# Performance work log

Hardware: AMD Instinct MI355X
Metric: run time of the kernel (lower is better)

Reference implementation:

```python
import jax, jax.numpy as jnp
import numpy as np

N = 8192
NFEAT = 512
NHID = 512
NCLASS = 64
NLAYERS = 8
LAMDA = 0.5
ALPHA = 0.1
EDGE_P = 0.002  # ~16 avg degree


def setup_inputs() -> dict:
    key = jax.random.key(0)
    ks = jax.random.split(key, 6)
    x = jax.random.normal(ks[0], (N, NFEAT), dtype=jnp.float32)
    # sparse 0/1 adjacency, densified (the original densifies adj each layer)
    adj = (jax.random.uniform(ks[1], (N, N)) < EDGE_P).astype(jnp.float32)
    stdv1 = 1.0 / np.sqrt(NHID)
    fc1_W = jax.random.normal(ks[2], (NFEAT, NHID), dtype=jnp.float32) * stdv1
    fc1_b = jnp.zeros((NHID,), dtype=jnp.float32)
    # GraphConvolution.reset_parameters: uniform(-1/sqrt(out), 1/sqrt(out))
    conv_Ws = jax.random.uniform(ks[3], (NLAYERS, NHID, NHID), minval=-stdv1, maxval=stdv1, dtype=jnp.float32)
    stdv2 = 1.0 / np.sqrt(NCLASS)
    fc2_W = jax.random.normal(ks[4], (NHID, NCLASS), dtype=jnp.float32) * stdv2
    fc2_b = jnp.zeros((NCLASS,), dtype=jnp.float32)
    return {"x": x, "adj": adj, "fc1_W": fc1_W, "fc1_b": fc1_b,
            "conv_Ws": conv_Ws, "fc2_W": fc2_W, "fc2_b": fc2_b}


def reference(x, adj, fc1_W, fc1_b, conv_Ws, fc2_W, fc2_b):
    n = adj.shape[0]
    # A_hat = A + I ; P = D^{-1/2} A_hat D^{-1/2}  (diag matmuls -> row/col scaling)
    A_hat = adj + jnp.eye(n, dtype=adj.dtype)
    dinv = 1.0 / jnp.sqrt(jnp.sum(A_hat, axis=0))  # [N]
    P = dinv[:, None] * A_hat * dinv[None, :]      # identical every layer; compute once

    H0 = jax.nn.relu(x @ fc1_W + fc1_b)            # fc1 (dropout is identity: training=False)
    H = H0
    for i in range(NLAYERS):
        beta = float(np.log(LAMDA / (i + 1) + 1.0))
        init_res = (1.0 - ALPHA) * (P @ H) + ALPHA * H0
        # init_res @ ((1-beta) I + beta W) expanded:
        H = jax.nn.relu((1.0 - beta) * init_res + beta * (init_res @ conv_Ws[i]))
    logits = H @ fc2_W + fc2_b
    return -jax.nn.log_softmax(logits, axis=1)
```

## Files before the change

kernel.cpp:

```cpp
#include <hip/hip_runtime.h>
#include <hip/hip_bf16.h>
#include <cmath>

#define N_NODES 8192
#define NFEAT 512
#define NHID 512
#define NCLASS 64
#define NLAYERS 8
#define CAP 96

typedef __attribute__((ext_vector_type(8))) short bf16x8;
typedef __attribute__((ext_vector_type(4))) float f32x4;
typedef unsigned short u16;

__device__ inline float bf2f(short u) {
  union { unsigned int i; float f; } x;
  x.i = ((unsigned int)(u16)u) << 16;
  return x.f;
}
__device__ inline short f2bf(float f) {
  union { float f; unsigned int i; } x;
  x.f = f;
  unsigned int r = x.i + 0x7FFFu + ((x.i >> 16) & 1u);
  return (short)(r >> 16);
}

__global__ __launch_bounds__(256)
void extract_kernel(const float* __restrict__ adj, int* __restrict__ idx,
                    int* __restrict__ cnt, int* __restrict__ colcnt)
{
  __shared__ int s_cnt;
  const int i = blockIdx.x;
  if (threadIdx.x == 0) s_cnt = 0;
  __syncthreads();
  const uint4* row = (const uint4*)(adj + (size_t)i * N_NODES);
  for (int c = threadIdx.x; c < N_NODES / 4; c += 256) {
    uint4 v = row[c];
    if ((v.x | v.y | v.z | v.w) == 0u) continue;
    unsigned int vals[4] = {v.x, v.y, v.z, v.w};
    #pragma unroll
    for (int e = 0; e < 4; ++e) {
      if (vals[e] != 0u) {
        int p = atomicAdd(&s_cnt, 1);
        if (p < CAP) idx[(size_t)i * CAP + p] = c * 4 + e;
        atomicAdd(&colcnt[c * 4 + e], 1);
      }
    }
  }
  __syncthreads();
  if (threadIdx.x == 0) cnt[i] = min(s_cnt, CAP);
}

__global__ __launch_bounds__(256)
void dinv_kernel(const int* __restrict__ colcnt, float* __restrict__ dinv)
{
  int j = blockIdx.x * 256 + threadIdx.x;
  if (j < N_NODES) dinv[j] = 1.0f / sqrtf((float)colcnt[j] + 1.0f);
}

__global__ __launch_bounds__(256)
void cvt_bf16_kernel(const float* __restrict__ src, u16* __restrict__ dst, int n4)
{
  int i = blockIdx.x * 256 + threadIdx.x;
  if (i >= n4) return;
  float4 v = ((const float4*)src)[i];
  ushort4 o;
  o.x = (u16)f2bf(v.x); o.y = (u16)f2bf(v.y);
  o.z = (u16)f2bf(v.z); o.w = (u16)f2bf(v.w);
  ((ushort4*)dst)[i] = o;
}

__global__ __launch_bounds__(256)
void transpose_cast_kernel(const float* __restrict__ fc1W, const float* __restrict__ convW,
                           u16* __restrict__ Wt)
{
  __shared__ float tile[32][33];
  const int m = blockIdx.z;
  const float* src = (m == 0) ? fc1W : convW + (size_t)(m - 1) * NHID * NHID;
  u16* dst = Wt + (size_t)m * NHID * NHID;
  const int k0 = blockIdx.x * 32, n0 = blockIdx.y * 32;
  const int tx = threadIdx.x & 31, ty = threadIdx.x >> 5;
  #pragma unroll
  for (int r = 0; r < 32; r += 8)
    tile[ty + r][tx] = src[(size_t)(k0 + ty + r) * NHID + n0 + tx];
  __syncthreads();
  #pragma unroll
  for (int r = 0; r < 32; r += 8)
    dst[(size_t)(n0 + ty + r) * NHID + k0 + tx] = (u16)f2bf(tile[tx][ty + r]);
}

#define AS1 __attribute__((address_space(1)))
#define AS3 __attribute__((address_space(3)))

__device__ inline void load16(const void* g, void* l) {
  __builtin_amdgcn_global_load_lds((const AS1 void*)g, (AS3 void*)l, 16, 0, 0);
}

template<int MODE>
__global__ __launch_bounds__(256, 2)
void gemm_kernel(const u16* __restrict__ A, const u16* __restrict__ Bt,
                 const float* __restrict__ bias, const u16* __restrict__ skip,
                 const float* __restrict__ dinv, float cA, float cB,
                 u16* __restrict__ out0, u16* __restrict__ out1)
{
  constexpr int K = 512, N = 512;
  __shared__ u16 ldsA[2][64 * 32];
  __shared__ u16 ldsB[2][128 * 32];
  const int tid = threadIdx.x;
  const int wave = tid >> 6, lane = tid & 63;
  const int m0 = blockIdx.x * 64, n0 = blockIdx.y * 128;
  const int wr = wave >> 1, wc = wave & 1;
  const int lrow = lane & 15, lk = lane >> 4;

  f32x4 acc[2][4];
  #pragma unroll
  for (int a = 0; a < 2; ++a)
    #pragma unroll
    for (int b = 0; b < 4; ++b)
      acc[a][b] = (f32x4){0.f, 0.f, 0.f, 0.f};

  auto stage = [&](int b, int ks) {
    {
      const int c = wave * 64 + lane;
      load16(A + (size_t)(m0 + (c >> 2)) * K + ks + (c & 3) * 8,
             &ldsA[b][(wave * 64) * 8]);
    }
    #pragma unroll
    for (int r = 0; r < 2; ++r) {
      const int c = r * 256 + wave * 64 + lane;
      load16(Bt + (size_t)(n0 + (c >> 2)) * K + ks + (c & 3) * 8,
             &ldsB[b][(r * 256 + wave * 64) * 8]);
    }
  };

  stage(0, 0);
  __syncthreads();

  for (int t = 0; t < 16; ++t) {
    const int b = t & 1;
    if (t + 1 < 16) stage(b ^ 1, (t + 1) * 32);
    bf16x8 af[2], bfr[4];
    #pragma unroll
    for (int mi = 0; mi < 2; ++mi)
      af[mi] = *(const bf16x8*)&ldsA[b][(wr * 32 + mi * 16 + lrow) * 32 + lk * 8];
    #pragma unroll
    for (int ni = 0; ni < 4; ++ni)
      bfr[ni] = *(const bf16x8*)&ldsB[b][(wc * 64 + ni * 16 + lrow) * 32 + lk * 8];
    #pragma unroll
    for (int mi = 0; mi < 2; ++mi)
      #pragma unroll
      for (int ni = 0; ni < 4; ++ni)
        acc[mi][ni] = __builtin_amdgcn_mfma_f32_16x16x32_bf16(af[mi], bfr[ni], acc[mi][ni], 0, 0, 0);
    __syncthreads();
  }

  #pragma unroll
  for (int mi = 0; mi < 2; ++mi) {
    #pragma unroll
    for (int ni = 0; ni < 4; ++ni) {
      #pragma unroll
      for (int r = 0; r < 4; ++r) {
        const int row = m0 + wr * 32 + mi * 16 + lk * 4 + r;
        const int col = n0 + wc * 64 + ni * 16 + lrow;
        const size_t o = (size_t)row * N + col;
        float v = acc[mi][ni][r];
        if (MODE == 0) {
          v = fmaxf(v + bias[col], 0.f);
          out0[o] = (u16)f2bf(v);
          out1[o] = (u16)f2bf(dinv[row] * v);
        } else {
          v = fmaxf(cA * bf2f((short)skip[o]) + cB * v, 0.f);
          out0[o] = (u16)f2bf(MODE == 1 ? dinv[row] * v : v);
        }
      }
    }
  }
}

__global__ __launch_bounds__(256)
void spmm_kernel(const u16* __restrict__ Hs, const u16* __restrict__ H0,
                 const float* __restrict__ dinv, const int* __restrict__ idx,
                 const int* __restrict__ cnt, u16* __restrict__ IR)
{
  const int wave = threadIdx.x >> 6, lane = threadIdx.x & 63;
  const int i = blockIdx.x * 4 + wave;
  const int c0 = lane * 8;
  const int n = cnt[i];
  int jreg = 0;
  if (lane < n) jreg = idx[(size_t)i * CAP + lane] & (N_NODES - 1);

  float acc[8];
  #pragma unroll
  for (int e = 0; e < 8; ++e) acc[e] = 0.f;

  const int nn = min(n, 64);
  int t = 0;
  for (; t + 8 <= nn; t += 8) {
    bf16x8 v[8];
    #pragma unroll
    for (int u = 0; u < 8; ++u) {
      const int j = __shfl(jreg, t + u);
      v[u] = *(const bf16x8*)&Hs[(size_t)j * NHID + c0];
    }
    #pragma unroll
    for (int u = 0; u < 8; ++u)
      #pragma unroll
      for (int e = 0; e < 8; ++e)
        acc[e] += bf2f(v[u][e]);
  }
  for (; t < nn; ++t) {
    const int j = __shfl(jreg, t);
    bf16x8 v = *(const bf16x8*)&Hs[(size_t)j * NHID + c0];
    #pragma unroll
    for (int e = 0; e < 8; ++e) acc[e] += bf2f(v[e]);
  }
  for (; t < n; ++t) {
    const int j = idx[(size_t)i * CAP + t] & (N_NODES - 1);
    bf16x8 v = *(const bf16x8*)&Hs[(size_t)j * NHID + c0];
    #pragma unroll
    for (int e = 0; e < 8; ++e) acc[e] += bf2f(v[e]);
  }

  const float di = dinv[i];
  bf16x8 self = *(const bf16x8*)&Hs[(size_t)i * NHID + c0];
  bf16x8 h0   = *(const bf16x8*)&H0[(size_t)i * NHID + c0];
  bf16x8 ov;
  #pragma unroll
  for (int e = 0; e < 8; ++e) {
    float v = 0.9f * di * (acc[e] + bf2f(self[e])) + 0.1f * bf2f(h0[e]);
    ov[e] = f2bf(v);
  }
  *(bf16x8*)&IR[(size_t)i * NHID + c0] = ov;
}

__global__ __launch_bounds__(256)
void fc2_softmax_kernel(const u16* __restrict__ H, const float* __restrict__ W,
                        const float* __restrict__ b, float* __restrict__ out)
{
  __shared__ float sh[4][4][512];
  const int wave = threadIdx.x >> 6, lane = threadIdx.x & 63;
  const int rowBase = blockIdx.x * 16 + wave * 4;
  #pragma unroll
  for (int rr = 0; rr < 4; ++rr) {
    bf16x8 hv = *(const bf16x8*)&H[(size_t)(rowBase + rr) * NHID + lane * 8];
    #pragma unroll
    for (int e = 0; e < 8; ++e) sh[wave][rr][lane * 8 + e] = bf2f(hv[e]);
  }
  __syncthreads();
  const float bb = b[lane];
  float a0 = bb, a1 = bb, a2 = bb, a3 = bb;
  #pragma unroll 8
  for (int k = 0; k < 512; ++k) {
    const float w = W[k * 64 + lane];
    a0 += sh[wave][0][k] * w;
    a1 += sh[wave][1][k] * w;
    a2 += sh[wave][2][k] * w;
    a3 += sh[wave][3][k] * w;
  }
  float accs[4] = {a0, a1, a2, a3};
  #pragma unroll
  for (int rr = 0; rr < 4; ++rr) {
    const float v = accs[rr];
    float mx = v;
    for (int off = 32; off > 0; off >>= 1) mx = fmaxf(mx, __shfl_xor(mx, off));
    float s = __expf(v - mx);
    for (int off = 32; off > 0; off >>= 1) s += __shfl_xor(s, off);
    out[(size_t)(rowBase + rr) * NCLASS + lane] = -(v - mx - logf(s));
  }
}

extern "C" void kernel_launch(void* const* d_in, const int* in_sizes, int n_in,
                              void* d_out, int out_size, void* d_ws, size_t ws_size,
                              hipStream_t stream)
{
  const float* x     = (const float*)d_in[0];
  const float* adj   = (const float*)d_in[1];
  const float* fc1W  = (const float*)d_in[2];
  const float* fc1b  = (const float*)d_in[3];
  const float* convW = (const float*)d_in[4];
  const float* fc2W  = (const float*)d_in[5];
  const float* fc2b  = (const float*)d_in[6];
  float* out = (float*)d_out;

  char* ws = (char*)d_ws;
  size_t off = 0;
  auto alloc = [&](size_t bytes) -> void* {
    void* p = ws + off;
    off = (off + bytes + 255) & ~(size_t)255;
    return p;
  };
  u16*   xb   = (u16*)alloc((size_t)N_NODES * NFEAT * 2);
  u16*   Wt   = (u16*)alloc((size_t)9 * NHID * NHID * 2);
  u16*   H0   = (u16*)alloc((size_t)N_NODES * NHID * 2);
  u16*   HsA  = (u16*)alloc((size_t)N_NODES * NHID * 2);
  u16*   HsB  = (u16*)alloc((size_t)N_NODES * NHID * 2);
  u16*   IR   = (u16*)alloc((size_t)N_NODES * NHID * 2);
  int*   idx  = (int*)alloc((size_t)N_NODES * CAP * 4);
  int*   cnt  = (int*)alloc((size_t)N_NODES * 4);
  int*   colc = (int*)alloc((size_t)N_NODES * 4);
  float* dinv = (float*)alloc((size_t)N_NODES * 4);

  hipMemsetAsync(colc, 0, N_NODES * 4, stream);
  extract_kernel<<<N_NODES, 256, 0, stream>>>(adj, idx, cnt, colc);
  dinv_kernel<<<N_NODES / 256, 256, 0, stream>>>(colc, dinv);
  cvt_bf16_kernel<<<(N_NODES * NFEAT / 4) / 256, 256, 0, stream>>>(x, xb, N_NODES * NFEAT / 4);
  transpose_cast_kernel<<<dim3(16, 16, 9), 256, 0, stream>>>(fc1W, convW, Wt);

  gemm_kernel<0><<<dim3(128, 4), 256, 0, stream>>>(xb, Wt, fc1b, nullptr, dinv, 0.f, 0.f, H0, HsA);

  const u16* Hin = HsA;
  for (int i = 0; i < NLAYERS; ++i) {
    const double beta = log(0.5 / (double)(i + 1) + 1.0);
    const float cA = (float)(1.0 - beta), cB = (float)beta;
    spmm_kernel<<<N_NODES / 4, 256, 0, stream>>>(Hin, H0, dinv, idx, cnt, IR);
    u16* Hout = (Hin == HsA) ? HsB : HsA;
    if (i < NLAYERS - 1)
      gemm_kernel<1><<<dim3(128, 4), 256, 0, stream>>>(
          IR, Wt + (size_t)(i + 1) * NHID * NHID, nullptr, IR, dinv, cA, cB, Hout, nullptr);
    else
      gemm_kernel<2><<<dim3(128, 4), 256, 0, stream>>>(
          IR, Wt + (size_t)(i + 1) * NHID * NHID, nullptr, IR, dinv, cA, cB, Hout, nullptr);
    Hin = Hout;
  }

  fc2_softmax_kernel<<<N_NODES / 16, 256, 0, stream>>>((const u16*)Hin, fc2W, fc2b, out);
}
```

Measured before the change: 361.8 us.

## Fold residual blend into weights, retile GEMM with swizzled LDS, fuse fc2 via MFMA

The (1-beta)I + beta*W blend is folded into the transposed bf16 conv weights, so the GEMM epilogue no longer reads the skip tensor. The GEMM changes from 64x128 tiles with K-step 32 to 64x64 tiles with K-step 64, using an XOR-swizzled shared-memory layout, a grouped block ordering and higher occupancy (4 blocks per SM). The scalar fc2+log_softmax kernel is replaced by an MFMA GEMM mode that does the log-softmax in its epilogue. Folding the identity into bf16 weights changes rounding slightly, and smaller tiles lower per-block data reuse.

```diff
diff --git a/kernel.cpp b/kernel.cpp
--- a/kernel.cpp
+++ b/kernel.cpp
@@ -70,23 +70,43 @@
   ((ushort4*)dst)[i] = o;
 }
 
+struct Coefs { float cA[8]; float cB[8]; };
+
 __global__ __launch_bounds__(256)
 void transpose_cast_kernel(const float* __restrict__ fc1W, const float* __restrict__ convW,
-                           u16* __restrict__ Wt)
+                           const float* __restrict__ fc2W,
+                           u16* __restrict__ Wt, u16* __restrict__ Wt2, Coefs co)
 {
   __shared__ float tile[32][33];
   const int m = blockIdx.z;
+  const int k0 = blockIdx.x * 32, n0 = blockIdx.y * 32;
+  if (m == 9 && n0 >= 64) return;
+  const int tx = threadIdx.x & 31, ty = threadIdx.x >> 5;
+  if (m == 9) {
+    #pragma unroll
+    for (int r = 0; r < 32; r += 8)
+      tile[ty + r][tx] = fc2W[(size_t)(k0 + ty + r) * 64 + n0 + tx];
+    __syncthreads();
+    #pragma unroll
+    for (int r = 0; r < 32; r += 8)
+      Wt2[(size_t)(n0 + ty + r) * 512 + k0 + tx] = (u16)f2bf(tile[tx][ty + r]);
+    return;
+  }
   const float* src = (m == 0) ? fc1W : convW + (size_t)(m - 1) * NHID * NHID;
   u16* dst = Wt + (size_t)m * NHID * NHID;
-  const int k0 = blockIdx.x * 32, n0 = blockIdx.y * 32;
-  const int tx = threadIdx.x & 31, ty = threadIdx.x >> 5;
+  float cA = 0.f, cB = 1.f;
+  if (m >= 1) { cA = co.cA[m - 1]; cB = co.cB[m - 1]; }
   #pragma unroll
   for (int r = 0; r < 32; r += 8)
     tile[ty + r][tx] = src[(size_t)(k0 + ty + r) * NHID + n0 + tx];
   __syncthreads();
   #pragma unroll
-  for (int r = 0; r < 32; r += 8)
-    dst[(size_t)(n0 + ty + r) * NHID + k0 + tx] = (u16)f2bf(tile[tx][ty + r]);
+  for (int r = 0; r < 32; r += 8) {
+    const int krow = k0 + tx, ncol = n0 + ty + r;
+    float val = cB * tile[tx][ty + r];
+    if (m >= 1 && krow == ncol) val += cA;
+    dst[(size_t)ncol * NHID + krow] = (u16)f2bf(val);
+  }
 }
 
 #define AS1 __attribute__((address_space(1)))
@@ -97,82 +117,128 @@
 }
 
 template<int MODE>
-__global__ __launch_bounds__(256, 2)
+__global__ __launch_bounds__(256, 4)
 void gemm_kernel(const u16* __restrict__ A, const u16* __restrict__ Bt,
-                 const float* __restrict__ bias, const u16* __restrict__ skip,
-                 const float* __restrict__ dinv, float cA, float cB,
-                 u16* __restrict__ out0, u16* __restrict__ out1)
-{
-  constexpr int K = 512, N = 512;
-  __shared__ u16 ldsA[2][64 * 32];
-  __shared__ u16 ldsB[2][128 * 32];
+                 const float* __restrict__ bias, const float* __restrict__ dinv,
+                 u16* __restrict__ out0, u16* __restrict__ out1,
+                 float* __restrict__ outF)
+{
+  constexpr int K = 512;
+  constexpr int N = (MODE == 3) ? NCLASS : 512;
+  __shared__ u16 lds[2][2][64 * 64];
   const int tid = threadIdx.x;
   const int wave = tid >> 6, lane = tid & 63;
-  const int m0 = blockIdx.x * 64, n0 = blockIdx.y * 128;
+
+  const int cpx = gridDim.x >> 3;
+  const int logical = (blockIdx.x & 7) * cpx + (blockIdx.x >> 3);
+  const int mblk = (MODE == 3) ? logical : (logical >> 3);
+  const int nblk = (MODE == 3) ? 0 : (logical & 7);
+  const int m0 = mblk * 64, n0 = nblk * 64;
+
   const int wr = wave >> 1, wc = wave & 1;
   const int lrow = lane & 15, lk = lane >> 4;
 
-  f32x4 acc[2][4];
+  f32x4 acc[2][2];
   #pragma unroll
   for (int a = 0; a < 2; ++a)
     #pragma unroll
-    for (int b = 0; b < 4; ++b)
+    for (int b = 0; b < 2; ++b)
       acc[a][b] = (f32x4){0.f, 0.f, 0.f, 0.f};
 
   auto stage = [&](int b, int ks) {
-    {
-      const int c = wave * 64 + lane;
-      load16(A + (size_t)(m0 + (c >> 2)) * K + ks + (c & 3) * 8,
-             &ldsA[b][(wave * 64) * 8]);
-    }
     #pragma unroll
     for (int r = 0; r < 2; ++r) {
       const int c = r * 256 + wave * 64 + lane;
-      load16(Bt + (size_t)(n0 + (c >> 2)) * K + ks + (c & 3) * 8,
-             &ldsB[b][(r * 256 + wave * 64) * 8]);
+      const int row = c >> 3;
+      const int sc = (c & 7) ^ (row & 7);
+      load16(A  + (size_t)(m0 + row) * K + ks + sc * 8, &lds[b][0][(r * 256 + wave * 64) * 8]);
+      load16(Bt + (size_t)(n0 + row) * K + ks + sc * 8, &lds[b][1][(r * 256 + wave * 64) * 8]);
     }
   };
 
   stage(0, 0);
   __syncthreads();
 
-  for (int t = 0; t < 16; ++t) {
+  for (int t = 0; t < 8; ++t) {
     const int b = t & 1;
-    if (t + 1 < 16) stage(b ^ 1, (t + 1) * 32);
-    bf16x8 af[2], bfr[4];
-    #pragma unroll
-    for (int mi = 0; mi < 2; ++mi)
-      af[mi] = *(const bf16x8*)&ldsA[b][(wr * 32 + mi * 16 + lrow) * 32 + lk * 8];
-    #pragma unroll
-    for (int ni = 0; ni < 4; ++ni)
-      bfr[ni] = *(const bf16x8*)&ldsB[b][(wc * 64 + ni * 16 + lrow) * 32 + lk * 8];
-    #pragma unroll
-    for (int mi = 0; mi < 2; ++mi)
-      #pragma unroll
-      for (int ni = 0; ni < 4; ++ni)
-        acc[mi][ni] = __builtin_amdgcn_mfma_f32_16x16x32_bf16(af[mi], bfr[ni], acc[mi][ni], 0, 0, 0);
+    if (t + 1 < 8) stage(b ^ 1, (t + 1) * 64);
+    const char* pA = (const char*)lds[b][0];
+    const char* pB = (const char*)lds[b][1];
+    bf16x8 af[2][2], bfr[2][2];
+    #pragma unroll
+    for (int mi = 0; mi < 2; ++mi) {
+      const int row = wr * 32 + mi * 16 + lrow;
+      #pragma unroll
+      for (int ks2 = 0; ks2 < 2; ++ks2) {
+        const int j = ks2 * 4 + lk;
+        af[mi][ks2] = *(const bf16x8*)(pA + row * 128 + ((j ^ (row & 7)) * 16));
+      }
+    }
+    #pragma unroll
+    for (int ni = 0; ni < 2; ++ni) {
+      const int row = wc * 32 + ni * 16 + lrow;
+      #pragma unroll
+      for (int ks2 = 0; ks2 < 2; ++ks2) {
+        const int j = ks2 * 4 + lk;
+        bfr[ni][ks2] = *(const bf16x8*)(pB + row * 128 + ((j ^ (row & 7)) * 16));
+      }
+    }
+    #pragma unroll
+    for (int ks2 = 0; ks2 < 2; ++ks2)
+      #pragma unroll
+      for (int mi = 0; mi < 2; ++mi)
+        #pragma unroll
+        for (int ni = 0; ni < 2; ++ni)
+          acc[mi][ni] = __builtin_amdgcn_mfma_f32_16x16x32_bf16(af[mi][ks2], bfr[ni][ks2], acc[mi][ni], 0, 0, 0);
     __syncthreads();
   }
 
-  #pragma unroll
-  for (int mi = 0; mi < 2; ++mi) {
-    #pragma unroll
-    for (int ni = 0; ni < 4; ++ni) {
-      #pragma unroll
-      for (int r = 0; r < 4; ++r) {
-        const int row = m0 + wr * 32 + mi * 16 + lk * 4 + r;
-        const int col = n0 + wc * 64 + ni * 16 + lrow;
-        const size_t o = (size_t)row * N + col;
-        float v = acc[mi][ni][r];
-        if (MODE == 0) {
-          v = fmaxf(v + bias[col], 0.f);
-          out0[o] = (u16)f2bf(v);
-          out1[o] = (u16)f2bf(dinv[row] * v);
-        } else {
-          v = fmaxf(cA * bf2f((short)skip[o]) + cB * v, 0.f);
-          out0[o] = (u16)f2bf(MODE == 1 ? dinv[row] * v : v);
+  if (MODE != 3) {
+    #pragma unroll
+    for (int mi = 0; mi < 2; ++mi) {
+      #pragma unroll
+      for (int ni = 0; ni < 2; ++ni) {
+        #pragma unroll
+        for (int r = 0; r < 4; ++r) {
+          const int row = m0 + wr * 32 + mi * 16 + lk * 4 + r;
+          const int col = n0 + wc * 32 + ni * 16 + lrow;
+          const size_t o = (size_t)row * N + col;
+          float v = acc[mi][ni][r];
+          if (MODE == 0) {
+            v = fmaxf(v + bias[col], 0.f);
+            out0[o] = (u16)f2bf(v);
+            out1[o] = (u16)f2bf(dinv[row] * v);
+          } else {
+            v = fmaxf(v, 0.f);
+            out0[o] = (u16)f2bf(MODE == 1 ? dinv[row] * v : v);
+          }
         }
       }
+    }
+  } else {
+    float* Cf = (float*)&lds[0][0][0];
+    #pragma unroll
+    for (int mi = 0; mi < 2; ++mi)
+      #pragma unroll
+      for (int ni = 0; ni < 2; ++ni)
+        #pragma unroll
+        for (int r = 0; r < 4; ++r) {
+          const int row = wr * 32 + mi * 16 + lk * 4 + r;
+          const int col = wc * 32 + ni * 16 + lrow;
+          Cf[row * 65 + col] = acc[mi][ni][r] + bias[col];
+        }
+    __syncthreads();
+    #pragma unroll 4
+    for (int r = 0; r < 16; ++r) {
+      const int row = wave * 16 + r;
+      const float v = Cf[row * 65 + lane];
+      float mx = v;
+      #pragma unroll
+      for (int off = 32; off > 0; off >>= 1) mx = fmaxf(mx, __shfl_xor(mx, off));
+      float s = __expf(v - mx);
+      #pragma unroll
+      for (int off = 32; off > 0; off >>= 1) s += __shfl_xor(s, off);
+      outF[(size_t)(m0 + row) * NCLASS + lane] = -(v - mx - logf(s));
     }
   }
 }
@@ -231,42 +297,6 @@
     ov[e] = f2bf(v);
   }
   *(bf16x8*)&IR[(size_t)i * NHID + c0] = ov;
-}
-
-__global__ __launch_bounds__(256)
-void fc2_softmax_kernel(const u16* __restrict__ H, const float* __restrict__ W,
-                        const float* __restrict__ b, float* __restrict__ out)
-{
-  __shared__ float sh[4][4][512];
-  const int wave = threadIdx.x >> 6, lane = threadIdx.x & 63;
-  const int rowBase = blockIdx.x * 16 + wave * 4;
-  #pragma unroll
-  for (int rr = 0; rr < 4; ++rr) {
-    bf16x8 hv = *(const bf16x8*)&H[(size_t)(rowBase + rr) * NHID + lane * 8];
-    #pragma unroll
-    for (int e = 0; e < 8; ++e) sh[wave][rr][lane * 8 + e] = bf2f(hv[e]);
-  }
-  __syncthreads();
-  const float bb = b[lane];
-  float a0 = bb, a1 = bb, a2 = bb, a3 = bb;
-  #pragma unroll 8
-  for (int k = 0; k < 512; ++k) {
-    const float w = W[k * 64 + lane];
-    a0 += sh[wave][0][k] * w;
-    a1 += sh[wave][1][k] * w;
-    a2 += sh[wave][2][k] * w;
-    a3 += sh[wave][3][k] * w;
-  }
-  float accs[4] = {a0, a1, a2, a3};
-  #pragma unroll
-  for (int rr = 0; rr < 4; ++rr) {
-    const float v = accs[rr];
-    float mx = v;
-    for (int off = 32; off > 0; off >>= 1) mx = fmaxf(mx, __shfl_xor(mx, off));
-    float s = __expf(v - mx);
-    for (int off = 32; off > 0; off >>= 1) s += __shfl_xor(s, off);
-    out[(size_t)(rowBase + rr) * NCLASS + lane] = -(v - mx - logf(s));
-  }
 }
 
 extern "C" void kernel_launch(void* const* d_in, const int* in_sizes, int n_in,
@@ -291,6 +321,7 @@
   };
   u16*   xb   = (u16*)alloc((size_t)N_NODES * NFEAT * 2);
   u16*   Wt   = (u16*)alloc((size_t)9 * NHID * NHID * 2);
+  u16*   Wt2  = (u16*)alloc((size_t)NCLASS * NHID * 2);
   u16*   H0   = (u16*)alloc((size_t)N_NODES * NHID * 2);
   u16*   HsA  = (u16*)alloc((size_t)N_NODES * NHID * 2);
   u16*   HsB  = (u16*)alloc((size_t)N_NODES * NHID * 2);
@@ -300,28 +331,33 @@
   int*   colc = (int*)alloc((size_t)N_NODES * 4);
   float* dinv = (float*)alloc((size_t)N_NODES * 4);
 
+  Coefs co;
+  for (int i = 0; i < NLAYERS; ++i) {
+    const double beta = log(0.5 / (double)(i + 1) + 1.0);
+    co.cA[i] = (float)(1.0 - beta);
+    co.cB[i] = (float)beta;
+  }
+
   hipMemsetAsync(colc, 0, N_NODES * 4, stream);
   extract_kernel<<<N_NODES, 256, 0, stream>>>(adj, idx, cnt, colc);
   dinv_kernel<<<N_NODES / 256, 256, 0, stream>>>(colc, dinv);
   cvt_bf16_kernel<<<(N_NODES * NFEAT / 4) / 256, 256, 0, stream>>>(x, xb, N_NODES * NFEAT / 4);
-  transpose_cast_kernel<<<dim3(16, 16, 9), 256, 0, stream>>>(fc1W, convW, Wt);
-
-  gemm_kernel<0><<<dim3(128, 4), 256, 0, stream>>>(xb, Wt, fc1b, nullptr, dinv, 0.f, 0.f, H0, HsA);
+  transpose_cast_kernel<<<dim3(16, 16, 10), 256, 0, stream>>>(fc1W, convW, fc2W, Wt, Wt2, co);
+
+  gemm_kernel<0><<<1024, 256, 0, stream>>>(xb, Wt, fc1b, dinv, H0, HsA, nullptr);
 
   const u16* Hin = HsA;
   for (int i = 0; i < NLAYERS; ++i) {
-    const double beta = log(0.5 / (double)(i + 1) + 1.0);
-    const float cA = (float)(1.0 - beta), cB = (float)beta;
     spmm_kernel<<<N_NODES / 4, 256, 0, stream>>>(Hin, H0, dinv, idx, cnt, IR);
     u16* Hout = (Hin == HsA) ? HsB : HsA;
     if (i < NLAYERS - 1)
-      gemm_kernel<1><<<dim3(128, 4), 256, 0, stream>>>(
-          IR, Wt + (size_t)(i + 1) * NHID * NHID, nullptr, IR, dinv, cA, cB, Hout, nullptr);
+      gemm_kernel<1><<<1024, 256, 0, stream>>>(
+          IR, Wt + (size_t)(i + 1) * NHID * NHID, nullptr, dinv, Hout, nullptr, nullptr);
     else
-      gemm_kernel<2><<<dim3(128, 4), 256, 0, stream>>>(
-          IR, Wt + (size_t)(i + 1) * NHID * NHID, nullptr, IR, dinv, cA, cB, Hout, nullptr);
+      gemm_kernel<2><<<1024, 256, 0, stream>>>(
+          IR, Wt + (size_t)(i + 1) * NHID * NHID, nullptr, dinv, Hout, nullptr, nullptr);
     Hin = Hout;
   }
 
-  fc2_softmax_kernel<<<N_NODES / 16, 256, 0, stream>>>((const u16*)Hin, fc2W, fc2b, out);
-}
+  gemm_kernel<3><<<128, 256, 0, stream>>>((const u16*)Hin, Wt2, fc2b, nullptr, nullptr, nullptr, out);
+}
```

Result: faster. 305.3 us (-15.6%).
